# Kernel tuning notes

Hardware: AMD Instinct MI355X
Metric: run time of the kernel (lower is better)

The kernel has to match this reference:

```python
import jax, jax.numpy as jnp
import numpy as np


def setup_inputs() -> dict:
    key = jax.random.key(0)
    ks = jax.random.split(key, 5)
    B, H, W, KV = 32, 32, 32, 1024
    N, K, V = 16, 64, 64
    return {
        "key_value": jax.random.normal(ks[0], (B, H, W, KV), dtype=jnp.float32),
        "query": jax.random.normal(ks[1], (1, 1, N, K), dtype=jnp.float32),
        "k_kernel": jax.random.normal(ks[2], (KV, N * K), dtype=jnp.float32) * 0.03,
        "k_bias": jnp.zeros((N * K,), dtype=jnp.float32),
        "v_kernel": jax.random.normal(ks[3], (KV, N * V), dtype=jnp.float32) * 0.03,
        "v_bias": jnp.zeros((N * V,), dtype=jnp.float32),
    }


def reference(key_value, query, k_kernel, k_bias, v_kernel, v_bias):
    # key_value: [B,H,W,KV]; 1x1 conv == channel GEMM
    B, H, W, KV = key_value.shape
    N, K = query.shape[2], query.shape[3]
    V = v_kernel.shape[1] // N
    x = key_value.reshape(B, H * W, KV)                      # [B,HW,KV]
    k = (x @ k_kernel + k_bias).reshape(B, H * W, N, K)       # [B,HW,N,K]
    v = (x @ v_kernel + v_bias).reshape(B, H * W, N, V)       # [B,HW,N,V]
    # single-query dot product per head (no 1/sqrt(K) scaling, per original)
    logits = jnp.einsum('bsnk,nk->bsn', k, query[0, 0])       # [B,HW,N]
    attn = jax.nn.softmax(logits, axis=1)                     # softmax over HW
    out = jnp.einsum('bsn,bsnv->bnv', attn, v)                # [B,N,V]
    return out
```

## Files before the change

### kernel.cpp

```cpp
#include <hip/hip_runtime.h>
#include <hip/hip_fp16.h>


__device__ __forceinline__ float rlane(float v, int l) {
  return __int_as_float(__builtin_amdgcn_readlane(__float_as_int(v), l));
}

__global__ __launch_bounds__(256) void k_qk(const float* __restrict__ kk,
                                            const float* __restrict__ q,
                                            const float* __restrict__ kb,
                                            float* __restrict__ qk,
                                            float* __restrict__ qb) {
  const int gid = blockIdx.x * 256 + threadIdx.x;
  const int c = gid >> 4, n = gid & 15;
  float a = 0.f;
#pragma unroll
  for (int k4 = 0; k4 < 64; k4 += 4) {
    const float4 kv = *(const float4*)(kk + (size_t)c * 1024 + n * 64 + k4);
    const float4 qv = *(const float4*)(q + n * 64 + k4);
    a += kv.x * qv.x + kv.y * qv.y + kv.z * qv.z + kv.w * qv.w;
  }
  qk[gid] = a;
  if (blockIdx.x == 0 && threadIdx.x < 16) {
    float s = 0.f;
    for (int k = 0; k < 64; k++) s += kb[threadIdx.x * 64 + k] * q[threadIdx.x * 64 + k];
    qb[threadIdx.x] = s;
  }
}

__global__ __launch_bounds__(512, 4) void k_fused(const float* __restrict__ x,
                                                  const float* __restrict__ qk,
                                                  const float* __restrict__ qb,
                                                  float* __restrict__ mch,
                                                  float* __restrict__ lch,
                                                  __half* __restrict__ wph) {
  __shared__ float qkt[16384];
  __shared__ float et2[64 * 17 + 4];
  const int tid = threadIdx.x;
  const int lane = tid & 63;
  const int wid = tid >> 6;
  const int blk = blockIdx.x;
  const int srow0 = blk * 64;

#pragma unroll
  for (int it = 0; it < 8; ++it) {
    const int g = it * 512 + tid;
    const float4 v = *(const float4*)(qk + (size_t)g * 4);
    *(float4*)&qkt[(g & 3) * 4096 + (g >> 2) * 4] = v;
  }
  __syncthreads();

#pragma unroll 1
  for (int sweep = 0; sweep < 2; ++sweep) {
    const int rloc = sweep * 32 + wid * 4;
    const float* xw = x + (size_t)(srow0 + rloc) * 1024 + lane;

    float acc[4][16];
#pragma unroll
    for (int r = 0; r < 4; ++r)
#pragma unroll
      for (int n = 0; n < 16; ++n) acc[r][n] = 0.f;

    float xa[4], xb[4];
#pragma unroll
    for (int r = 0; r < 4; ++r) xa[r] = xw[(size_t)r * 1024];

#pragma unroll 1
    for (int st = 0; st < 16; st += 2) {
#pragma unroll
      for (int r = 0; r < 4; ++r) xb[r] = xw[(size_t)r * 1024 + (st + 1) * 64];
      {
        const int c4 = (st * 64 + lane) * 4;
#pragma unroll
        for (int nq = 0; nq < 4; ++nq) {
          const float4 qv = *(const float4*)&qkt[nq * 4096 + c4];
#pragma unroll
          for (int r = 0; r < 4; ++r) {
            acc[r][nq * 4 + 0] += xa[r] * qv.x;
            acc[r][nq * 4 + 1] += xa[r] * qv.y;
            acc[r][nq * 4 + 2] += xa[r] * qv.z;
            acc[r][nq * 4 + 3] += xa[r] * qv.w;
          }
        }
      }
      if (st + 2 < 16) {
#pragma unroll
        for (int r = 0; r < 4; ++r) xa[r] = xw[(size_t)r * 1024 + (st + 2) * 64];
      }
      {
        const int c4 = ((st + 1) * 64 + lane) * 4;
#pragma unroll
        for (int nq = 0; nq < 4; ++nq) {
          const float4 qv = *(const float4*)&qkt[nq * 4096 + c4];
#pragma unroll
          for (int r = 0; r < 4; ++r) {
            acc[r][nq * 4 + 0] += xb[r] * qv.x;
            acc[r][nq * 4 + 1] += xb[r] * qv.y;
            acc[r][nq * 4 + 2] += xb[r] * qv.z;
            acc[r][nq * 4 + 3] += xb[r] * qv.w;
          }
        }
      }
    }

    const int b0 = lane & 1, b1 = (lane >> 1) & 1;
    const int b2 = (lane >> 2) & 1, b3 = (lane >> 3) & 1;
    float f[4];
#pragma unroll
    for (int r = 0; r < 4; ++r) {
      float u[8];
#pragma unroll
      for (int m = 0; m < 8; ++m) {
        const float keep = b0 ? acc[r][2 * m + 1] : acc[r][2 * m];
        const float give = b0 ? acc[r][2 * m]     : acc[r][2 * m + 1];
        u[m] = keep + __shfl_xor(give, 1);
      }
      float w[4];
#pragma unroll
      for (int p = 0; p < 4; ++p) {
        const float keep = b1 ? u[2 * p + 1] : u[2 * p];
        const float give = b1 ? u[2 * p]     : u[2 * p + 1];
        w[p] = keep + __shfl_xor(give, 2);
      }
      float z[2];
#pragma unroll
      for (int qq = 0; qq < 2; ++qq) {
        const float keep = b2 ? w[2 * qq + 1] : w[2 * qq];
        const float give = b2 ? w[2 * qq]     : w[2 * qq + 1];
        z[qq] = keep + __shfl_xor(give, 4);
      }
      {
        const float keep = b3 ? z[1] : z[0];
        const float give = b3 ? z[0] : z[1];
        float t = keep + __shfl_xor(give, 8);
        t += __shfl_xor(t, 16);
        t += __shfl_xor(t, 32);
        f[r] = t;
      }
    }
    const int rsel = lane >> 4;
    float val = (rsel == 0) ? f[0] : (rsel == 1) ? f[1] : (rsel == 2) ? f[2] : f[3];
    val += qb[lane & 15];
    et2[(rloc + rsel) * 17 + (lane & 15)] = val;
  }
  __syncthreads();

#pragma unroll
  for (int t = 0; t < 2; ++t) {
    const int nn = wid + t * 8;
    const float v = et2[lane * 17 + nn];
    float m = v;
#pragma unroll
    for (int d = 1; d < 64; d <<= 1) m = fmaxf(m, __shfl_xor(m, d));
    const float e = __expf(v - m);
    float s = e;
#pragma unroll
    for (int d = 1; d < 64; d <<= 1) s += __shfl_xor(s, d);
    if (lane == 0) {
      mch[blk * 16 + nn] = m;
      lch[blk * 16 + nn] = s;
    }
    et2[lane * 17 + nn] = e;
  }
  __syncthreads();

  {
    const int c0 = wid * 128 + lane;
    float acc0[16], acc1[16];
#pragma unroll
    for (int n = 0; n < 16; ++n) { acc0[n] = 0.f; acc1[n] = 0.f; }
    const float* xp = x + (size_t)srow0 * 1024;

    float e4 = et2[(lane >> 4) * 17 + (lane & 15)];
    float x0[4], x1[4];
#pragma unroll
    for (int ss = 0; ss < 4; ++ss) {
      x0[ss] = xp[(size_t)ss * 1024 + c0];
      x1[ss] = xp[(size_t)ss * 1024 + c0 + 64];
    }
#pragma unroll 1
    for (int sg = 0; sg < 16; ++sg) {
      float e4n = 0.f, x0n[4], x1n[4];
      if (sg < 15) {
        const int s0n = (sg + 1) * 4;
        e4n = et2[(s0n + (lane >> 4)) * 17 + (lane & 15)];
#pragma unroll
        for (int ss = 0; ss < 4; ++ss) {
          x0n[ss] = xp[(size_t)(s0n + ss) * 1024 + c0];
          x1n[ss] = xp[(size_t)(s0n + ss) * 1024 + c0 + 64];
        }
      }
#pragma unroll
      for (int ss = 0; ss < 4; ++ss) {
#pragma unroll
        for (int n = 0; n < 16; ++n) {
          const float ev = rlane(e4, ss * 16 + n);
          acc0[n] += ev * x0[ss];
          acc1[n] += ev * x1[ss];
        }
      }
      e4 = e4n;
#pragma unroll
      for (int ss = 0; ss < 4; ++ss) { x0[ss] = x0n[ss]; x1[ss] = x1n[ss]; }
    }

    __half* wpp = wph + (size_t)blk * 16384;
#pragma unroll
    for (int n = 0; n < 16; ++n) {
      wpp[n * 1024 + c0]      = __float2half(acc0[n]);
      wpp[n * 1024 + c0 + 64] = __float2half(acc1[n]);
    }
  }
}

__global__ __launch_bounds__(256) void k_out(const __half* __restrict__ wph,
                                             const float* __restrict__ vk,
                                             const float* __restrict__ vb,
                                             const float* __restrict__ mch,
                                             const float* __restrict__ lch,
                                             float* __restrict__ out) {
  const int bi = blockIdx.x;
  const int b = bi >> 4, n = bi & 15;
  const int tid = threadIdx.x;
  __shared__ float wrow[1024];
  __shared__ float red[4][64];

  float m16[16], l16[16];
#pragma unroll
  for (int ch = 0; ch < 16; ++ch) {
    m16[ch] = mch[(b * 16 + ch) * 16 + n];
    l16[ch] = lch[(b * 16 + ch) * 16 + n];
  }
  float mg = m16[0];
#pragma unroll
  for (int ch = 1; ch < 16; ++ch) mg = fmaxf(mg, m16[ch]);
  float fac[16], lg = 0.f;
#pragma unroll
  for (int ch = 0; ch < 16; ++ch) { fac[ch] = __expf(m16[ch] - mg); lg += fac[ch] * l16[ch]; }

  float4 a4 = {0.f, 0.f, 0.f, 0.f};
#pragma unroll
  for (int ch = 0; ch < 16; ch++) {
    const __half2* p = (const __half2*)(wph + ((size_t)(b * 16 + ch) * 16 + n) * 1024 + tid * 4);
    const float2 f01 = __half22float2(p[0]);
    const float2 f23 = __half22float2(p[1]);
    a4.x += fac[ch] * f01.x; a4.y += fac[ch] * f01.y;
    a4.z += fac[ch] * f23.x; a4.w += fac[ch] * f23.y;
  }
  *(float4*)&wrow[tid * 4] = a4;
  __syncthreads();

  const int v = tid & 63, cq = tid >> 6;
  float a = 0.f;
  const float* vkc = vk + n * 64 + v;
  for (int ci = 0; ci < 256; ci++) {
    const int c = cq * 256 + ci;
    a += wrow[c] * vkc[(size_t)c * 1024];
  }
  red[cq][v] = a;
  __syncthreads();
  if (tid < 64) {
    const float o = (red[0][tid] + red[1][tid] + red[2][tid] + red[3][tid]) / lg
                    + vb[n * 64 + tid];
    out[(size_t)b * 1024 + n * 64 + tid] = o;
  }
}

extern "C" void kernel_launch(void* const* d_in, const int* in_sizes, int n_in,
                              void* d_out, int out_size, void* d_ws, size_t ws_size,
                              hipStream_t stream) {
  const float* x  = (const float*)d_in[0];
  const float* q  = (const float*)d_in[1];
  const float* kk = (const float*)d_in[2];
  const float* kb = (const float*)d_in[3];
  const float* vk = (const float*)d_in[4];
  const float* vb = (const float*)d_in[5];
  float* out = (float*)d_out;

  float*  f   = (float*)d_ws;
  float*  qk  = f;
  float*  qb  = f + 16384;
  float*  mch = f + 16400;
  float*  lch = f + 24592;
  __half* wph = (__half*)(f + 32784);

  hipLaunchKernelGGL(k_qk,    dim3(64),  dim3(256), 0, stream, kk, q, kb, qk, qb);
  hipLaunchKernelGGL(k_fused, dim3(512), dim3(512), 0, stream, x, qk, qb, mch, lch, wph);
  hipLaunchKernelGGL(k_out,   dim3(512), dim3(256), 0, stream, wph, vk, vb, mch, lch, out);
}
```

Measured before the change: 68.94 us.

## Vectorize x loads as float2 with interleaved qk layout and deeper prefetch

Changes the layout of the precomputed qk table so adjacent channel pairs are interleaved. The logits GEMM and the weighted-sum phase can then read x as float2 per lane and write the fp16 partials as half2. Both loops are fully unrolled with a two-stage-ahead register prefetch buffer, replacing the earlier single-step double buffering. This cuts the number of global load instructions and aims to hide more latency, at the cost of higher register pressure, which may reduce occupancy or cause spills under the 512x4 launch bound.

```diff
diff --git a/kernel.cpp b/kernel.cpp
--- a/kernel.cpp
+++ b/kernel.cpp
@@ -9,7 +9,7 @@
 __global__ __launch_bounds__(256) void k_qk(const float* __restrict__ kk,
                                             const float* __restrict__ q,
                                             const float* __restrict__ kb,
-                                            float* __restrict__ qk,
+                                            float* __restrict__ qk2,
                                             float* __restrict__ qb) {
   const int gid = blockIdx.x * 256 + threadIdx.x;
   const int c = gid >> 4, n = gid & 15;
@@ -20,7 +20,7 @@
     const float4 qv = *(const float4*)(q + n * 64 + k4);
     a += kv.x * qv.x + kv.y * qv.y + kv.z * qv.z + kv.w * qv.w;
   }
-  qk[gid] = a;
+  qk2[(n >> 2) * 4096 + (c >> 1) * 8 + (c & 1) * 4 + (n & 3)] = a;
   if (blockIdx.x == 0 && threadIdx.x < 16) {
     float s = 0.f;
     for (int k = 0; k < 64; k++) s += kb[threadIdx.x * 64 + k] * q[threadIdx.x * 64 + k];
@@ -29,7 +29,7 @@
 }
 
 __global__ __launch_bounds__(512, 4) void k_fused(const float* __restrict__ x,
-                                                  const float* __restrict__ qk,
+                                                  const float* __restrict__ qk2,
                                                   const float* __restrict__ qb,
                                                   float* __restrict__ mch,
                                                   float* __restrict__ lch,
@@ -45,15 +45,14 @@
 #pragma unroll
   for (int it = 0; it < 8; ++it) {
     const int g = it * 512 + tid;
-    const float4 v = *(const float4*)(qk + (size_t)g * 4);
-    *(float4*)&qkt[(g & 3) * 4096 + (g >> 2) * 4] = v;
+    *(float4*)&qkt[g * 4] = *(const float4*)(qk2 + (size_t)g * 4);
   }
   __syncthreads();
 
 #pragma unroll 1
   for (int sweep = 0; sweep < 2; ++sweep) {
     const int rloc = sweep * 32 + wid * 4;
-    const float* xw = x + (size_t)(srow0 + rloc) * 1024 + lane;
+    const float* xw = x + (size_t)(srow0 + rloc) * 1024 + 2 * lane;
 
     float acc[4][16];
 #pragma unroll
@@ -61,44 +60,32 @@
 #pragma unroll
       for (int n = 0; n < 16; ++n) acc[r][n] = 0.f;
 
-    float xa[4], xb[4];
-#pragma unroll
-    for (int r = 0; r < 4; ++r) xa[r] = xw[(size_t)r * 1024];
-
-#pragma unroll 1
-    for (int st = 0; st < 16; st += 2) {
-#pragma unroll
-      for (int r = 0; r < 4; ++r) xb[r] = xw[(size_t)r * 1024 + (st + 1) * 64];
-      {
-        const int c4 = (st * 64 + lane) * 4;
-#pragma unroll
-        for (int nq = 0; nq < 4; ++nq) {
-          const float4 qv = *(const float4*)&qkt[nq * 4096 + c4];
-#pragma unroll
-          for (int r = 0; r < 4; ++r) {
-            acc[r][nq * 4 + 0] += xa[r] * qv.x;
-            acc[r][nq * 4 + 1] += xa[r] * qv.y;
-            acc[r][nq * 4 + 2] += xa[r] * qv.z;
-            acc[r][nq * 4 + 3] += xa[r] * qv.w;
-          }
-        }
-      }
-      if (st + 2 < 16) {
-#pragma unroll
-        for (int r = 0; r < 4; ++r) xa[r] = xw[(size_t)r * 1024 + (st + 2) * 64];
-      }
-      {
-        const int c4 = ((st + 1) * 64 + lane) * 4;
-#pragma unroll
-        for (int nq = 0; nq < 4; ++nq) {
-          const float4 qv = *(const float4*)&qkt[nq * 4096 + c4];
-#pragma unroll
-          for (int r = 0; r < 4; ++r) {
-            acc[r][nq * 4 + 0] += xb[r] * qv.x;
-            acc[r][nq * 4 + 1] += xb[r] * qv.y;
-            acc[r][nq * 4 + 2] += xb[r] * qv.z;
-            acc[r][nq * 4 + 3] += xb[r] * qv.w;
-          }
+    float2 xbuf[8][4];
+#pragma unroll
+    for (int p = 0; p < 2; ++p)
+#pragma unroll
+      for (int r = 0; r < 4; ++r)
+        xbuf[p][r] = *(const float2*)(xw + (size_t)r * 1024 + p * 128);
+
+#pragma unroll
+    for (int st = 0; st < 8; ++st) {
+      if (st + 2 < 8) {
+#pragma unroll
+        for (int r = 0; r < 4; ++r)
+          xbuf[st + 2][r] = *(const float2*)(xw + (size_t)r * 1024 + (st + 2) * 128);
+      }
+      const int base = (st * 64 + lane) * 8;
+#pragma unroll
+      for (int nq = 0; nq < 4; ++nq) {
+        const float4 qe = *(const float4*)&qkt[nq * 4096 + base];
+        const float4 qo = *(const float4*)&qkt[nq * 4096 + base + 4];
+#pragma unroll
+        for (int r = 0; r < 4; ++r) {
+          const float x0 = xbuf[st][r].x, x1 = xbuf[st][r].y;
+          acc[r][nq * 4 + 0] += x0 * qe.x + x1 * qo.x;
+          acc[r][nq * 4 + 1] += x0 * qe.y + x1 * qo.y;
+          acc[r][nq * 4 + 2] += x0 * qe.z + x1 * qo.z;
+          acc[r][nq * 4 + 3] += x0 * qe.w + x1 * qo.w;
         }
       }
     }
@@ -165,50 +152,45 @@
   __syncthreads();
 
   {
-    const int c0 = wid * 128 + lane;
+    const int c0 = tid * 2;
     float acc0[16], acc1[16];
 #pragma unroll
     for (int n = 0; n < 16; ++n) { acc0[n] = 0.f; acc1[n] = 0.f; }
-    const float* xp = x + (size_t)srow0 * 1024;
-
-    float e4 = et2[(lane >> 4) * 17 + (lane & 15)];
-    float x0[4], x1[4];
-#pragma unroll
-    for (int ss = 0; ss < 4; ++ss) {
-      x0[ss] = xp[(size_t)ss * 1024 + c0];
-      x1[ss] = xp[(size_t)ss * 1024 + c0 + 64];
-    }
-#pragma unroll 1
+    const float* xp = x + (size_t)srow0 * 1024 + c0;
+
+    float2 xc[16][4];
+    float  e4[16];
+#pragma unroll
+    for (int p = 0; p < 2; ++p) {
+      e4[p] = et2[(p * 4 + (lane >> 4)) * 17 + (lane & 15)];
+#pragma unroll
+      for (int ss = 0; ss < 4; ++ss)
+        xc[p][ss] = *(const float2*)(xp + (size_t)(p * 4 + ss) * 1024);
+    }
+#pragma unroll
     for (int sg = 0; sg < 16; ++sg) {
-      float e4n = 0.f, x0n[4], x1n[4];
-      if (sg < 15) {
-        const int s0n = (sg + 1) * 4;
-        e4n = et2[(s0n + (lane >> 4)) * 17 + (lane & 15)];
-#pragma unroll
-        for (int ss = 0; ss < 4; ++ss) {
-          x0n[ss] = xp[(size_t)(s0n + ss) * 1024 + c0];
-          x1n[ss] = xp[(size_t)(s0n + ss) * 1024 + c0 + 64];
+      if (sg + 2 < 16) {
+        e4[sg + 2] = et2[((sg + 2) * 4 + (lane >> 4)) * 17 + (lane & 15)];
+#pragma unroll
+        for (int ss = 0; ss < 4; ++ss)
+          xc[sg + 2][ss] = *(const float2*)(xp + (size_t)((sg + 2) * 4 + ss) * 1024);
+      }
+#pragma unroll
+      for (int ss = 0; ss < 4; ++ss) {
+#pragma unroll
+        for (int n = 0; n < 16; ++n) {
+          const float ev = rlane(e4[sg], ss * 16 + n);
+          acc0[n] += ev * xc[sg][ss].x;
+          acc1[n] += ev * xc[sg][ss].y;
         }
       }
-#pragma unroll
-      for (int ss = 0; ss < 4; ++ss) {
-#pragma unroll
-        for (int n = 0; n < 16; ++n) {
-          const float ev = rlane(e4, ss * 16 + n);
-          acc0[n] += ev * x0[ss];
-          acc1[n] += ev * x1[ss];
-        }
-      }
-      e4 = e4n;
-#pragma unroll
-      for (int ss = 0; ss < 4; ++ss) { x0[ss] = x0n[ss]; x1[ss] = x1n[ss]; }
     }
 
     __half* wpp = wph + (size_t)blk * 16384;
 #pragma unroll
     for (int n = 0; n < 16; ++n) {
-      wpp[n * 1024 + c0]      = __float2half(acc0[n]);
-      wpp[n * 1024 + c0 + 64] = __float2half(acc1[n]);
+      __half2 h = __floats2half2_rn(acc0[n], acc1[n]);
+      *(__half2*)(wpp + n * 1024 + c0) = h;
     }
   }
 }
@@ -278,13 +260,13 @@
   float* out = (float*)d_out;
 
   float*  f   = (float*)d_ws;
-  float*  qk  = f;
+  float*  qk2 = f;
   float*  qb  = f + 16384;
   float*  mch = f + 16400;
   float*  lch = f + 24592;
   __half* wph = (__half*)(f + 32784);
 
-  hipLaunchKernelGGL(k_qk,    dim3(64),  dim3(256), 0, stream, kk, q, kb, qk, qb);
-  hipLaunchKernelGGL(k_fused, dim3(512), dim3(512), 0, stream, x, qk, qb, mch, lch, wph);
+  hipLaunchKernelGGL(k_qk,    dim3(64),  dim3(256), 0, stream, kk, q, kb, qk2, qb);
+  hipLaunchKernelGGL(k_fused, dim3(512), dim3(512), 0, stream, x, qk2, qb, mch, lch, wph);
   hipLaunchKernelGGL(k_out,   dim3(512), dim3(256), 0, stream, wph, vk, vb, mch, lch, out);
 }
```

Result: slower. 253.5 us (+267.7%).
